# Performance work log

Measured on AMD Instinct MI355X. Metric: run time of the kernel, lower is better.

## Reference

```python
import jax, jax.numpy as jnp
import numpy as np

B, C, H, W = 16, 256, 64, 64
K, HID, ITERS, EPS = 4, 512, 3, 1e-8


def _ln(x, g, b, eps=1e-5):
    m = jnp.mean(x, axis=-1, keepdims=True)
    v = jnp.mean((x - m) ** 2, axis=-1, keepdims=True)
    return (x - m) * jax.lax.rsqrt(v + eps) * g + b


def setup_inputs() -> dict:
    key = jax.random.key(0)
    ks = jax.random.split(key, 24)

    def lin(k, o, i):
        lim = np.sqrt(6.0 / (o + i)).astype(np.float32)
        return jax.random.uniform(k, (o, i), jnp.float32, -lim, lim)

    return {
        "x": jax.random.normal(ks[0], (B, C, H, W), jnp.float32),
        "noise": jax.random.normal(ks[1], (B, K, C), jnp.float32),
        "slot_mu": jax.random.normal(ks[2], (1, 1, C), jnp.float32),
        "slot_log_sigma": jnp.zeros((1, 1, C), jnp.float32),
        "ln_in_g": jnp.ones((C,)), "ln_in_b": jnp.zeros((C,)),
        "ln_sl_g": jnp.ones((C,)), "ln_sl_b": jnp.zeros((C,)),
        "ln_mlp_g": jnp.ones((C,)), "ln_mlp_b": jnp.zeros((C,)),
        "Wq": lin(ks[3], C, C), "bq": jnp.zeros((C,)),
        "Wk": lin(ks[4], C, C), "bk": jnp.zeros((C,)),
        "Wv": lin(ks[5], C, C), "bv": jnp.zeros((C,)),
        "Wu": lin(ks[6], C, 2 * C), "bu": jnp.zeros((C,)),
        "W1": lin(ks[7], HID, C), "b1": jnp.zeros((HID,)),
        "W2": lin(ks[8], C, HID), "b2": jnp.zeros((C,)),
        "We1": lin(ks[9], C // 2, C), "be1": jnp.zeros((C // 2,)),
        "We2": lin(ks[10], 1, C // 2), "be2": jnp.zeros((1,)),
    }


def reference(x, noise, slot_mu, slot_log_sigma, ln_in_g, ln_in_b, ln_sl_g, ln_sl_b,
              ln_mlp_g, ln_mlp_b, Wq, bq, Wk, bk, Wv, bv, Wu, bu, W1, b1, W2, b2,
              We1, be1, We2, be2):
    # b c h w -> b (h w) c
    xn = x.reshape(B, C, H * W).transpose(0, 2, 1)
    xn = _ln(xn, ln_in_g, ln_in_b)
    # k, v depend only on xn; hoisted out of the loop (same math)
    k = jnp.einsum('bnc,dc->bnd', xn, Wk) + bk
    v = jnp.einsum('bnc,dc->bnd', xn, Wv) + bv
    scale = C ** (-0.5)
    slots = slot_mu + jnp.exp(slot_log_sigma) * noise
    for _ in range(ITERS):
        prev = slots
        s = _ln(slots, ln_sl_g, ln_sl_b)
        q = jnp.einsum('bkc,dc->bkd', s, Wq) + bq
        attn = jax.nn.softmax(jnp.einsum('bkc,bnc->bkn', q, k) * scale, axis=1)
        w = attn / (jnp.sum(attn, axis=-1, keepdims=True) + EPS)
        updates = jnp.einsum('bkn,bnc->bkc', w, v)
        combined = jnp.concatenate([prev, updates], axis=-1)  # (B,K,2C)
        slots = jnp.einsum('bkc,dc->bkd', combined, Wu) + bu + prev
        m = _ln(slots, ln_mlp_g, ln_mlp_b)
        h = jax.nn.gelu(jnp.einsum('bkc,hc->bkh', m, W1) + b1, approximate=False)
        slots = slots + jnp.einsum('bkh,ch->bkc', h, W2) + b2
    e = jax.nn.gelu(jnp.einsum('bkc,dc->bkd', slots, We1) + be1, approximate=False)
    slot_weights = jax.nn.sigmoid(jnp.einsum('bkd,od->bko', e, We2) + be2)[..., 0]
    return slots, slot_weights
```

## Files before the change

kernel.cpp:

```cpp
#include <hip/hip_runtime.h>
#include <math.h>

#define B_    16
#define C_    256
#define NPIX  4096
#define K_    4
#define HID_  512
#define ITERS_ 3
#define NROWS (B_*NPIX)
#define EPS_  1e-8f

__device__ __forceinline__ float gelu_f(float x) {
    return 0.5f * x * (1.0f + erff(x * 0.70710678118654752f));
}

__device__ __forceinline__ unsigned short f2bf(float x) {
    union { float f; unsigned u; } v; v.f = x;
    unsigned r = v.u + 0x7fffu + ((v.u >> 16) & 1u);
    return (unsigned short)(r >> 16);
}
__device__ __forceinline__ float bflo(unsigned u) {
    union { unsigned u; float f; } v; v.u = u << 16; return v.f;
}
__device__ __forceinline__ float bfhi(unsigned u) {
    union { unsigned u; float f; } v; v.u = u & 0xffff0000u; return v.f;
}
__device__ __forceinline__ float4 shfl_xor4(float4 v, int m) {
    v.x = __shfl_xor(v.x, m); v.y = __shfl_xor(v.y, m);
    v.z = __shfl_xor(v.z, m); v.w = __shfl_xor(v.w, m);
    return v;
}
__device__ __forceinline__ void fma4(float4& a, const float4 w, const float4 s) {
    a.x = fmaf(w.x, s.x, a.x); a.y = fmaf(w.y, s.y, a.y);
    a.z = fmaf(w.z, s.z, a.z); a.w = fmaf(w.w, s.w, a.w);
}
__device__ __forceinline__ float hsum4(const float4 a) {
    return (a.x + a.y) + (a.z + a.w);
}

__device__ __forceinline__ void redpair256t(float a, float b, int t, float* r8,
                                            float& o1, float& o2) {
    #pragma unroll
    for (int m = 1; m <= 32; m <<= 1) { a += __shfl_xor(a, m); b += __shfl_xor(b, m); }
    if ((t & 63) == 0) { r8[(t >> 6) * 2] = a; r8[(t >> 6) * 2 + 1] = b; }
    __syncthreads();
    o1 = r8[0] + r8[2] + r8[4] + r8[6];
    o2 = r8[1] + r8[3] + r8[5] + r8[7];
}

__global__ __launch_bounds__(256) void prep_pack_kernel(
    const float* __restrict__ Wu, const float* __restrict__ W1,
    const float* __restrict__ W2, const float* __restrict__ We1,
    const float* __restrict__ Wq, const float* __restrict__ bk,
    const float* __restrict__ bq,
    float4* __restrict__ WuC4, float4* __restrict__ W14,
    float4* __restrict__ W24, float4* __restrict__ We14,
    float* __restrict__ wqoff) {
    __shared__ float r4[4];
    int i = blockIdx.x * 256 + threadIdx.x;
    if (blockIdx.x == 352) {
        int c = threadIdx.x;
        float s = 0.f;
        for (int dd = 0; dd < 256; ++dd) s = fmaf(Wq[dd * 256 + c], bk[dd], s);
        wqoff[c] = s;
        float p = bq[c] * bk[c];
        #pragma unroll
        for (int m = 1; m <= 32; m <<= 1) p += __shfl_xor(p, m);
        if ((c & 63) == 0) r4[c >> 6] = p;
        __syncthreads();
        if (c == 0) wqoff[256] = r4[0] + r4[1] + r4[2] + r4[3];
        return;
    }
    if (i < 16384) {
        int c4 = i >> 8, dd = i & 255;
        WuC4[i] = *(const float4*)&Wu[dd * 512 + c4 * 4];
    } else if (i < 49152) {
        int j = i - 16384; int c4 = j >> 9, h = j & 511;
        W14[j] = *(const float4*)&W1[h * 256 + c4 * 4];
    } else if (i < 81920) {
        int j = i - 49152; int h4 = j >> 8, dd = j & 255;
        W24[j] = *(const float4*)&W2[dd * 512 + h4 * 4];
    } else {
        int j = i - 81920; int c4 = j >> 7, e = j & 127;
        We14[j] = *(const float4*)&We1[e * 256 + c4 * 4];
    }
}

__global__ __launch_bounds__(256) void prep_compose_kernel(
    const float* __restrict__ Wu, const float* __restrict__ Wv,
    const float* __restrict__ Wk, const float* __restrict__ Wq,
    const float* __restrict__ bv, const float* __restrict__ bq,
    float4* __restrict__ WuC4, float4* __restrict__ Wqk4,
    float* __restrict__ bv2, float* __restrict__ bqk) {
    __shared__ float wur[256], wkc[256];
    __shared__ float ldsA[256], ldsB[256];
    __shared__ float r1[4], r2[4];
    const int d = blockIdx.x, c = threadIdx.x;
    wur[c] = Wu[d * 512 + 256 + c];
    wkc[c] = Wk[c * 256 + d];
    __syncthreads();
    float a = 0.f, b = 0.f;
    #pragma unroll 4
    for (int e = 0; e < 256; ++e) {
        a = fmaf(wur[e], Wv[e * 256 + c], a);
        b = fmaf(wkc[e], Wq[e * 256 + c], b);
    }
    ldsA[c] = a; ldsB[c] = b;
    float p1 = wur[c] * bv[c], p2 = wkc[c] * bq[c];
    #pragma unroll
    for (int m = 1; m <= 32; m <<= 1) { p1 += __shfl_xor(p1, m); p2 += __shfl_xor(p2, m); }
    if ((c & 63) == 0) { r1[c >> 6] = p1; r2[c >> 6] = p2; }
    __syncthreads();
    if (c < 64) {
        float4 qa = { ldsA[4 * c], ldsA[4 * c + 1], ldsA[4 * c + 2], ldsA[4 * c + 3] };
        float4 qb = { ldsB[4 * c], ldsB[4 * c + 1], ldsB[4 * c + 2], ldsB[4 * c + 3] };
        WuC4[(64 + c) * 256 + d] = qa;
        Wqk4[c * 256 + d] = qb;
    }
    if (c == 0) {
        bv2[d] = r1[0] + r1[1] + r1[2] + r1[3];
        bqk[d] = r2[0] + r2[1] + r2[2] + r2[3];
    }
}

__global__ __launch_bounds__(256) void xn_fused_kernel(
    const float* __restrict__ x, const float* __restrict__ g, const float* __restrict__ bta,
    unsigned short* __restrict__ xnb) {
    __shared__ float tile[256][65];
    __shared__ float sg[256], sb[256];
    __shared__ float red1[256], red2[256];
    __shared__ float smean[64], srstd[64];
    const int tid = threadIdx.x;
    const int nt = blockIdx.x << 6, b = blockIdx.y;

    sg[tid] = g[tid]; sb[tid] = bta[tid];
    #pragma unroll
    for (int r = 0; r < 64; ++r) {
        int idx = tid + (r << 8);
        int c_l = idx >> 6, n_l = idx & 63;
        tile[c_l][n_l] = x[(size_t)(b * C_ + c_l) * NPIX + nt + n_l];
    }
    __syncthreads();
    {
        int cq = tid >> 6, n_l = tid & 63;
        float s = 0.f, s2 = 0.f;
        #pragma unroll 8
        for (int c = cq * 64; c < cq * 64 + 64; ++c) {
            float v = tile[c][n_l];
            s += v; s2 += v * v;
        }
        red1[tid] = s; red2[tid] = s2;
    }
    __syncthreads();
    if (tid < 64) {
        float s  = red1[tid] + red1[tid + 64] + red1[tid + 128] + red1[tid + 192];
        float s2 = red2[tid] + red2[tid + 64] + red2[tid + 128] + red2[tid + 192];
        float m = s * (1.0f / C_);
        smean[tid] = m;
        srstd[tid] = rsqrtf(s2 * (1.0f / C_) - m * m + 1e-5f);
    }
    __syncthreads();
    #pragma unroll
    for (int r = 0; r < 32; ++r) {
        int idx = tid + (r << 8);
        int n_l = idx >> 7, cp = idx & 127;
        int c0 = cp << 1;
        float mn = smean[n_l], rs = srstd[n_l];
        float v0 = (tile[c0][n_l] - mn) * rs * sg[c0] + sb[c0];
        float v1 = (tile[c0 + 1][n_l] - mn) * rs * sg[c0 + 1] + sb[c0 + 1];
        ushort2 o; o.x = f2bf(v0); o.y = f2bf(v1);
        *reinterpret_cast<ushort2*>(&xnb[((size_t)(b * NPIX + nt + n_l)) * C_ + c0]) = o;
    }
}


__global__ __launch_bounds__(256) void init_slots_kernel(
    const float* __restrict__ noise, const float* __restrict__ mu,
    const float* __restrict__ log_sigma,
    float* __restrict__ slots, float* __restrict__ usum, float* __restrict__ denom) {
    int t = threadIdx.x, r = blockIdx.x;
    float v = mu[t] + expf(log_sigma[t]) * noise[r * C_ + t];
    slots[r * C_ + t] = v;
    usum[r * C_ + t] = 0.f;
    if (t == 0) denom[r] = 0.f;
}

__global__ __launch_bounds__(256) void qt_kernel(
    const float* __restrict__ src,
    const float* __restrict__ g_sl, const float* __restrict__ b_sl,
    const float4* __restrict__ Wqk4, const float* __restrict__ bqk,
    const float* __restrict__ wqoff,
    float* __restrict__ qtbuf, float* __restrict__ qoffbuf) {
    __shared__ __align__(16) float snorm[256];
    __shared__ float pq[256];
    __shared__ float r8[8];
    const int t = threadIdx.x, dq = blockIdx.x, r = blockIdx.y;
    float v = src[r * C_ + t];
    float sm, s2;
    redpair256t(v, v * v, t, r8, sm, s2);
    float mean = sm * (1.f / C_);
    float rs = rsqrtf(s2 * (1.f / C_) - mean * mean + 1e-5f);
    snorm[t] = (v - mean) * rs * g_sl[t] + b_sl[t];
    __syncthreads();
    const float4* sn4 = (const float4*)snorm;
    const int dloc = t & 63, ks = t >> 6;
    const int d = dq * 64 + dloc;
    {
        float4 a0 = {0,0,0,0}, a1 = {0,0,0,0};
        int c4b = ks << 4;
        #pragma unroll
        for (int i = 0; i < 16; i += 2) {
            fma4(a0, Wqk4[(c4b + i) * 256 + d], sn4[c4b + i]);
            fma4(a1, Wqk4[(c4b + i + 1) * 256 + d], sn4[c4b + i + 1]);
        }
        pq[ks * 64 + dloc] = hsum4(a0) + hsum4(a1);
    }
    __syncthreads();
    if (t < 64) {
        float s = pq[t] + pq[64 + t] + pq[128 + t] + pq[192 + t];
        qtbuf[r * C_ + dq * 64 + t] = s + bqk[dq * 64 + t];
    }
    if (dq == 0) {
        float p = snorm[t] * wqoff[t];
        #pragma unroll
        for (int m = 1; m <= 32; m <<= 1) p += __shfl_xor(p, m);
        if ((t & 63) == 0) r8[t >> 6] = p;
        __syncthreads();
        if (t == 0) qoffbuf[r] = r8[0] + r8[1] + r8[2] + r8[3] + wqoff[256];
    }
}

__global__ __launch_bounds__(256) void upd_wu_kernel(
    const float* __restrict__ slots, const float* __restrict__ usum,
    const float* __restrict__ denom,
    const float4* __restrict__ WuC4, const float* __restrict__ bu,
    const float* __restrict__ bv2,
    float* __restrict__ nvbuf) {
    __shared__ __align__(16) float comb[512];
    __shared__ float pq[256];
    __shared__ float sden, sscale;
    const int t = threadIdx.x, dq = blockIdx.x, r = blockIdx.y;
    if (t == 0) { float dv = denom[r]; sden = dv + EPS_; sscale = dv / (dv + EPS_); }
    comb[t] = slots[r * C_ + t];
    float uv = usum[r * C_ + t];
    __syncthreads();
    comb[256 + t] = uv / sden;
    __syncthreads();
    const float4* cb4 = (const float4*)comb;
    const int dloc = t & 31, ks = t >> 5;
    const int d = dq * 32 + dloc;
    {
        float4 a0 = {0,0,0,0}, a1 = {0,0,0,0};
        int c4b = ks << 4;
        #pragma unroll
        for (int i = 0; i < 16; i += 2) {
            fma4(a0, WuC4[(c4b + i) * 256 + d], cb4[c4b + i]);
            fma4(a1, WuC4[(c4b + i + 1) * 256 + d], cb4[c4b + i + 1]);
        }
        pq[ks * 32 + dloc] = hsum4(a0) + hsum4(a1);
    }
    __syncthreads();
    if (t < 32) {
        int dd = dq * 32 + t;
        float s = 0.f;
        #pragma unroll
        for (int i = 0; i < 8; ++i) s += pq[i * 32 + t];
        nvbuf[r * C_ + dd] = s + bu[dd] + comb[dd] + sscale * bv2[dd];
    }
}

__global__ __launch_bounds__(256) void upd_w1_kernel(
    const float* __restrict__ nvbuf,
    const float* __restrict__ g_mlp, const float* __restrict__ b_mlp,
    const float4* __restrict__ W14, const float* __restrict__ b1,
    float* __restrict__ hbuf, float* __restrict__ usum, float* __restrict__ denom) {
    __shared__ __align__(16) float mrow[256];
    __shared__ float pq[256];
    __shared__ float r8[8];
    const int t = threadIdx.x, hq = blockIdx.x, r = blockIdx.y;
    float nv = nvbuf[r * C_ + t];
    float sm, s2;
    redpair256t(nv, nv * nv, t, r8, sm, s2);
    float mean = sm * (1.f / C_);
    float rs = rsqrtf(s2 * (1.f / C_) - mean * mean + 1e-5f);
    mrow[t] = (nv - mean) * rs * g_mlp[t] + b_mlp[t];
    if (hq == 0) {
        usum[r * C_ + t] = 0.f;
        if (t == 0) denom[r] = 0.f;
    }
    __syncthreads();
    const float4* m4 = (const float4*)mrow;
    const int hloc = t & 63, ks = t >> 6;
    const int h = hq * 64 + hloc;
    {
        float4 a0 = {0,0,0,0}, a1 = {0,0,0,0};
        int c4b = ks << 4;
        #pragma unroll
        for (int i = 0; i < 16; i += 2) {
            fma4(a0, W14[(c4b + i) * 512 + h], m4[c4b + i]);
            fma4(a1, W14[(c4b + i + 1) * 512 + h], m4[c4b + i + 1]);
        }
        pq[ks * 64 + hloc] = hsum4(a0) + hsum4(a1);
    }
    __syncthreads();
    if (t < 64) {
        float s = pq[t] + pq[64 + t] + pq[128 + t] + pq[192 + t];
        hbuf[r * HID_ + hq * 64 + t] = gelu_f(s + b1[hq * 64 + t]);
    }
}

__global__ __launch_bounds__(256) void upd_w2_kernel(
    const float* __restrict__ nvbuf, const float* __restrict__ hbuf,
    const float4* __restrict__ W24, const float* __restrict__ b2,
    float* __restrict__ dst) {
    __shared__ __align__(16) float hrow[512];
    __shared__ float pq[256];
    const int t = threadIdx.x, dq = blockIdx.x, r = blockIdx.y;
    hrow[t] = hbuf[r * HID_ + t];
    hrow[256 + t] = hbuf[r * HID_ + 256 + t];
    __syncthreads();
    const float4* h4 = (const float4*)hrow;
    const int dloc = t & 31, ks = t >> 5;
    const int d = dq * 32 + dloc;
    {
        float4 a0 = {0,0,0,0}, a1 = {0,0,0,0};
        int h4b = ks << 4;
        #pragma unroll
        for (int i = 0; i < 16; i += 2) {
            fma4(a0, W24[(h4b + i) * 256 + d], h4[h4b + i]);
            fma4(a1, W24[(h4b + i + 1) * 256 + d], h4[h4b + i + 1]);
        }
        pq[ks * 32 + dloc] = hsum4(a0) + hsum4(a1);
    }
    __syncthreads();
    if (t < 32) {
        int dd = dq * 32 + t;
        float s = 0.f;
        #pragma unroll
        for (int i = 0; i < 8; ++i) s += pq[i * 32 + t];
        dst[r * C_ + dd] = nvbuf[r * C_ + dd] + s + b2[dd];
    }
}

__global__ __launch_bounds__(256) void head_kernel(
    const float* __restrict__ ovbuf,
    const float4* __restrict__ We14, const float* __restrict__ be1,
    const float* __restrict__ We2, const float* __restrict__ be2,
    float* __restrict__ out) {
    __shared__ __align__(16) float mrow[256];
    __shared__ float pq[256];
    __shared__ float erow[128];
    __shared__ float r4[4];
    const int t = threadIdx.x, r = blockIdx.x;
    mrow[t] = ovbuf[r * C_ + t];
    __syncthreads();
    const float4* m4 = (const float4*)mrow;
    const int e = t & 127, o2 = t >> 7;
    {
        float4 a0 = {0,0,0,0}, a1 = {0,0,0,0};
        int c4b = o2 << 5;
        #pragma unroll
        for (int i = 0; i < 32; i += 2) {
            fma4(a0, We14[(c4b + i) * 128 + e], m4[c4b + i]);
            fma4(a1, We14[(c4b + i + 1) * 128 + e], m4[c4b + i + 1]);
        }
        pq[o2 * 128 + e] = hsum4(a0) + hsum4(a1);
    }
    __syncthreads();
    if (t < 128) erow[t] = gelu_f(pq[t] + pq[128 + t] + be1[t]);
    __syncthreads();
    if (t < 64) {
        float p = We2[t] * erow[t] + We2[t + 64] * erow[t + 64];
        #pragma unroll
        for (int m = 1; m <= 32; m <<= 1) p += __shfl_xor(p, m);
        if (t == 0) { r4[0] = p; }
    }
    __syncthreads();
    if (t == 0) out[B_ * K_ * C_ + r] = 1.0f / (1.0f + expf(-(r4[0] + be2[0])));
}

__global__ __launch_bounds__(256) void attn_fused_kernel(
    const float* __restrict__ qtbuf, const float* __restrict__ qoffbuf,
    const unsigned short* __restrict__ xnb,
    float* __restrict__ usum, float* __restrict__ denom) {
    __shared__ float4 qT[264];
    __shared__ float attns[K_][64];
    __shared__ float upd_s[K_][256];
    __shared__ float asw[4][4];
    __shared__ float4 qo_s;

    const int tid = threadIdx.x;
    const int b = blockIdx.y;
    const int chunk = blockIdx.x;
    const int n0 = chunk << 6;
    const int wave = tid >> 6, lane = tid & 63;

    {
        int c = tid;
        float4 qv;
        qv.x = qtbuf[b * 1024 + c];
        qv.y = qtbuf[b * 1024 + 256 + c];
        qv.z = qtbuf[b * 1024 + 512 + c];
        qv.w = qtbuf[b * 1024 + 768 + c];
        qT[c + (c >> 5)] = qv;
        if (tid == 0) qo_s = *(const float4*)&qoffbuf[b * 4];
    }
    __syncthreads();

    const int cpart = tid & 7;
    const int npair = tid >> 3;
    const int c0 = cpart << 5;
    float4 acc0 = {0.f, 0.f, 0.f, 0.f}, acc1 = {0.f, 0.f, 0.f, 0.f};
    const unsigned short* kbase = xnb + ((size_t)b * NPIX + n0 + npair * 2) * C_ + c0;
    #pragma unroll
    for (int j = 0; j < 4; ++j) {
        uint4 k0 = *reinterpret_cast<const uint4*>(kbase + j * 8);
        uint4 k1 = *reinterpret_cast<const uint4*>(kbase + C_ + j * 8);
        const unsigned kw0[4] = {k0.x, k0.y, k0.z, k0.w};
        const unsigned kw1[4] = {k1.x, k1.y, k1.z, k1.w};
        #pragma unroll
        for (int jj = 0; jj < 4; ++jj) {
            int cidx = c0 + j * 8 + jj * 2 + cpart;
            float4 qa = qT[cidx];
            float4 qb = qT[cidx + 1];
            float f00 = bflo(kw0[jj]), f01 = bfhi(kw0[jj]);
            float f10 = bflo(kw1[jj]), f11 = bfhi(kw1[jj]);
            acc0.x += f00 * qa.x + f01 * qb.x;  acc0.y += f00 * qa.y + f01 * qb.y;
            acc0.z += f00 * qa.z + f01 * qb.z;  acc0.w += f00 * qa.w + f01 * qb.w;
            acc1.x += f10 * qa.x + f11 * qb.x;  acc1.y += f10 * qa.y + f11 * qb.y;
            acc1.z += f10 * qa.z + f11 * qb.z;  acc1.w += f10 * qa.w + f11 * qb.w;
        }
    }
    #pragma unroll
    for (int m = 1; m <= 4; m <<= 1) {
        acc0 = acc0 + shfl_xor4(acc0, m);
        acc1 = acc1 + shfl_xor4(acc1, m);
    }
    float4 w0, w1;
    {
        float4 l = (acc0 + qo_s) * 0.0625f;
        float mx = fmaxf(fmaxf(l.x, l.y), fmaxf(l.z, l.w));
        w0.x = expf(l.x - mx); w0.y = expf(l.y - mx);
        w0.z = expf(l.z - mx); w0.w = expf(l.w - mx);
        float inv = 1.0f / (w0.x + w0.y + w0.z + w0.w);
        w0 = w0 * inv;
        l = (acc1 + qo_s) * 0.0625f;
        mx = fmaxf(fmaxf(l.x, l.y), fmaxf(l.z, l.w));
        w1.x = expf(l.x - mx); w1.y = expf(l.y - mx);
        w1.z = expf(l.z - mx); w1.w = expf(l.w - mx);
        inv = 1.0f / (w1.x + w1.y + w1.z + w1.w);
        w1 = w1 * inv;
    }
    if (cpart == 0) {
        int n_l = npair * 2;
        attns[0][n_l] = w0.x; attns[1][n_l] = w0.y; attns[2][n_l] = w0.z; attns[3][n_l] = w0.w;
        attns[0][n_l + 1] = w1.x; attns[1][n_l + 1] = w1.y;
        attns[2][n_l + 1] = w1.z; attns[3][n_l + 1] = w1.w;
    }
    float4 ws = w0 + w1;
    #pragma unroll
    for (int m = 8; m <= 32; m <<= 1) ws = ws + shfl_xor4(ws, m);
    if (lane == 0) {
        asw[wave][0] = ws.x; asw[wave][1] = ws.y; asw[wave][2] = ws.z; asw[wave][3] = ws.w;
    }
    __syncthreads();
    if (tid < 4)
        atomicAdd(&denom[b * 4 + tid],
                  asw[0][tid] + asw[1][tid] + asw[2][tid] + asw[3][tid]);

    const int h = wave >> 1;
    const int chalf = (wave & 1) << 7;
    const int c = chalf + lane * 2;
    float a0[K_] = {0.f, 0.f, 0.f, 0.f};
    float a1[K_] = {0.f, 0.f, 0.f, 0.f};
    const unsigned short* vbase = xnb + ((size_t)b * NPIX + n0 + h * 32) * C_ + c;
    #pragma unroll 4
    for (int nn = 0; nn < 32; ++nn) {
        unsigned vv = *reinterpret_cast<const unsigned*>(vbase + (size_t)nn * C_);
        float v0 = bflo(vv), v1 = bfhi(vv);
        int n_l = h * 32 + nn;
        float q0 = attns[0][n_l], q1 = attns[1][n_l], q2 = attns[2][n_l], q3 = attns[3][n_l];
        a0[0] = fmaf(q0, v0, a0[0]); a1[0] = fmaf(q0, v1, a1[0]);
        a0[1] = fmaf(q1, v0, a0[1]); a1[1] = fmaf(q1, v1, a1[1]);
        a0[2] = fmaf(q2, v0, a0[2]); a1[2] = fmaf(q2, v1, a1[2]);
        a0[3] = fmaf(q3, v0, a0[3]); a1[3] = fmaf(q3, v1, a1[3]);
    }
    __syncthreads();
    if (h == 0) {
        #pragma unroll
        for (int k = 0; k < K_; ++k) { upd_s[k][c] = a0[k]; upd_s[k][c + 1] = a1[k]; }
    }
    __syncthreads();
    if (h == 1) {
        #pragma unroll
        for (int k = 0; k < K_; ++k) { upd_s[k][c] += a0[k]; upd_s[k][c + 1] += a1[k]; }
    }
    __syncthreads();
    #pragma unroll
    for (int k = 0; k < K_; ++k)
        atomicAdd(&usum[((size_t)b * K_ + k) * 256 + tid], upd_s[k][tid]);
}

extern "C" void kernel_launch(void* const* d_in, const int* in_sizes, int n_in,
                              void* d_out, int out_size, void* d_ws, size_t ws_size,
                              hipStream_t stream) {
    (void)in_sizes; (void)n_in; (void)out_size; (void)ws_size;
    const float* x        = (const float*)d_in[0];
    const float* noise    = (const float*)d_in[1];
    const float* slot_mu  = (const float*)d_in[2];
    const float* slot_ls  = (const float*)d_in[3];
    const float* ln_in_g  = (const float*)d_in[4];
    const float* ln_in_b  = (const float*)d_in[5];
    const float* ln_sl_g  = (const float*)d_in[6];
    const float* ln_sl_b  = (const float*)d_in[7];
    const float* ln_mlp_g = (const float*)d_in[8];
    const float* ln_mlp_b = (const float*)d_in[9];
    const float* Wq = (const float*)d_in[10];
    const float* bq = (const float*)d_in[11];
    const float* Wk = (const float*)d_in[12];
    const float* bk = (const float*)d_in[13];
    const float* Wv = (const float*)d_in[14];
    const float* bv = (const float*)d_in[15];
    const float* Wu = (const float*)d_in[16];
    const float* bu = (const float*)d_in[17];
    const float* W1 = (const float*)d_in[18];
    const float* b1 = (const float*)d_in[19];
    const float* W2 = (const float*)d_in[20];
    const float* b2 = (const float*)d_in[21];
    const float* We1 = (const float*)d_in[22];
    const float* be1 = (const float*)d_in[23];
    const float* We2 = (const float*)d_in[24];
    const float* be2 = (const float*)d_in[25];
    float* out = (float*)d_out;

    char* ws = (char*)d_ws;
    unsigned short* xnb = (unsigned short*)ws;
    float4* WuC4 = (float4*)(xnb + (size_t)NROWS * C_);
    float4* W14  = WuC4 + 32768;
    float4* W24  = W14 + 32768;
    float4* We14 = W24 + 32768;
    float4* Wqk4 = We14 + 8192;
    float* bv2   = (float*)(Wqk4 + 16384);
    float* bqk   = bv2 + 256;
    float* wqoff = bqk + 256;
    float* slots = wqoff + 260;
    float* qtbuf = slots + B_ * K_ * C_;
    float* qoffb = qtbuf + B_ * K_ * C_;
    float* usum  = qoffb + B_ * K_;
    float* denom = usum + B_ * K_ * C_;
    float* nvbuf = denom + B_ * K_;
    float* hbuf  = nvbuf + B_ * K_ * C_;

    prep_pack_kernel<<<353, 256, 0, stream>>>(Wu, W1, W2, We1, Wq, bk, bq,
                                              WuC4, W14, W24, We14, wqoff);
    prep_compose_kernel<<<256, 256, 0, stream>>>(Wu, Wv, Wk, Wq, bv, bq,
                                                 WuC4, Wqk4, bv2, bqk);
    xn_fused_kernel<<<dim3(64, 16), 256, 0, stream>>>(x, ln_in_g, ln_in_b, xnb);
    init_slots_kernel<<<B_ * K_, 256, 0, stream>>>(noise, slot_mu, slot_ls,
                                                   slots, usum, denom);
    qt_kernel<<<dim3(4, B_ * K_), 256, 0, stream>>>(slots, ln_sl_g, ln_sl_b,
                                                    Wqk4, bqk, wqoff, qtbuf, qoffb);
    for (int it = 0; it < ITERS_; ++it) {
        attn_fused_kernel<<<dim3(64, 16), 256, 0, stream>>>(qtbuf, qoffb, xnb,
                                                            usum, denom);
        upd_wu_kernel<<<dim3(8, B_ * K_), 256, 0, stream>>>(slots, usum, denom,
                                                            WuC4, bu, bv2, nvbuf);
        upd_w1_kernel<<<dim3(8, B_ * K_), 256, 0, stream>>>(nvbuf, ln_mlp_g, ln_mlp_b,
                                                            W14, b1, hbuf, usum, denom);
        upd_w2_kernel<<<dim3(8, B_ * K_), 256, 0, stream>>>(
            nvbuf, hbuf, W24, b2, (it < ITERS_ - 1) ? slots : out);
        if (it < ITERS_ - 1)
            qt_kernel<<<dim3(4, B_ * K_), 256, 0, stream>>>(slots, ln_sl_g, ln_sl_b,
                                                            Wqk4, bqk, wqoff, qtbuf, qoffb);
    }
    head_kernel<<<B_ * K_, 256, 0, stream>>>(out, We14, be1, We2, be2, out);
}
```

Measured before the change: 299.0 us.

## Fuse slot-update chain into one kernel, merge prep kernels, retile attention and LN

Merges the two weight-prep kernels into one launch and folds slot init into the first q-projection kernel. Replaces the per-iteration Wu/W1/W2/qt/head kernel chain with a single upd_full kernel that does the update, MLP, next query and final head. It double-buffers slots and usum/denom so the accumulators can be cleared without racing. The attention kernel now runs on half as many blocks, each looping over more pixels. The input layernorm uses 512 threads and accumulates its statistics while loading. This cuts launch count and intermediate global round-trips, but each fused block recomputes the update redundantly across 2 blocks and uses less parallelism per row.

```diff
diff --git a/kernel.cpp b/kernel.cpp
--- a/kernel.cpp
+++ b/kernel.cpp
@@ -48,54 +48,53 @@
     o2 = r8[1] + r8[3] + r8[5] + r8[7];
 }
 
-__global__ __launch_bounds__(256) void prep_pack_kernel(
+__global__ __launch_bounds__(256) void prep_all_kernel(
     const float* __restrict__ Wu, const float* __restrict__ W1,
     const float* __restrict__ W2, const float* __restrict__ We1,
-    const float* __restrict__ Wq, const float* __restrict__ bk,
-    const float* __restrict__ bq,
+    const float* __restrict__ Wq, const float* __restrict__ Wk,
+    const float* __restrict__ Wv,
+    const float* __restrict__ bk, const float* __restrict__ bq,
+    const float* __restrict__ bv,
     float4* __restrict__ WuC4, float4* __restrict__ W14,
     float4* __restrict__ W24, float4* __restrict__ We14,
-    float* __restrict__ wqoff) {
-    __shared__ float r4[4];
-    int i = blockIdx.x * 256 + threadIdx.x;
-    if (blockIdx.x == 352) {
-        int c = threadIdx.x;
-        float s = 0.f;
-        for (int dd = 0; dd < 256; ++dd) s = fmaf(Wq[dd * 256 + c], bk[dd], s);
-        wqoff[c] = s;
-        float p = bq[c] * bk[c];
-        #pragma unroll
-        for (int m = 1; m <= 32; m <<= 1) p += __shfl_xor(p, m);
-        if ((c & 63) == 0) r4[c >> 6] = p;
-        __syncthreads();
-        if (c == 0) wqoff[256] = r4[0] + r4[1] + r4[2] + r4[3];
+    float4* __restrict__ Wqk4,
+    float* __restrict__ bv2, float* __restrict__ bqk, float* __restrict__ wqoff) {
+    const int role = blockIdx.x;
+    if (role < 353) {
+        __shared__ float r4[4];
+        if (role == 352) {
+            int c = threadIdx.x;
+            float s = 0.f;
+            for (int dd = 0; dd < 256; ++dd) s = fmaf(Wq[dd * 256 + c], bk[dd], s);
+            wqoff[c] = s;
+            float p = bq[c] * bk[c];
+            #pragma unroll
+            for (int m = 1; m <= 32; m <<= 1) p += __shfl_xor(p, m);
+            if ((c & 63) == 0) r4[c >> 6] = p;
+            __syncthreads();
+            if (c == 0) wqoff[256] = r4[0] + r4[1] + r4[2] + r4[3];
+            return;
+        }
+        int i = role * 256 + threadIdx.x;
+        if (i < 16384) {
+            int c4 = i >> 8, dd = i & 255;
+            WuC4[i] = *(const float4*)&Wu[dd * 512 + c4 * 4];
+        } else if (i < 49152) {
+            int j = i - 16384; int c4 = j >> 9, h = j & 511;
+            W14[j] = *(const float4*)&W1[h * 256 + c4 * 4];
+        } else if (i < 81920) {
+            int j = i - 49152; int h4 = j >> 8, dd = j & 255;
+            W24[j] = *(const float4*)&W2[dd * 512 + h4 * 4];
+        } else {
+            int j = i - 81920; int c4 = j >> 7, e = j & 127;
+            We14[j] = *(const float4*)&We1[e * 256 + c4 * 4];
+        }
         return;
     }
-    if (i < 16384) {
-        int c4 = i >> 8, dd = i & 255;
-        WuC4[i] = *(const float4*)&Wu[dd * 512 + c4 * 4];
-    } else if (i < 49152) {
-        int j = i - 16384; int c4 = j >> 9, h = j & 511;
-        W14[j] = *(const float4*)&W1[h * 256 + c4 * 4];
-    } else if (i < 81920) {
-        int j = i - 49152; int h4 = j >> 8, dd = j & 255;
-        W24[j] = *(const float4*)&W2[dd * 512 + h4 * 4];
-    } else {
-        int j = i - 81920; int c4 = j >> 7, e = j & 127;
-        We14[j] = *(const float4*)&We1[e * 256 + c4 * 4];
-    }
-}
-
-__global__ __launch_bounds__(256) void prep_compose_kernel(
-    const float* __restrict__ Wu, const float* __restrict__ Wv,
-    const float* __restrict__ Wk, const float* __restrict__ Wq,
-    const float* __restrict__ bv, const float* __restrict__ bq,
-    float4* __restrict__ WuC4, float4* __restrict__ Wqk4,
-    float* __restrict__ bv2, float* __restrict__ bqk) {
     __shared__ float wur[256], wkc[256];
     __shared__ float ldsA[256], ldsB[256];
     __shared__ float r1[4], r2[4];
-    const int d = blockIdx.x, c = threadIdx.x;
+    const int d = role - 353, c = threadIdx.x;
     wur[c] = Wu[d * 512 + 256 + c];
     wkc[c] = Wk[c * 256 + d];
     __syncthreads();
@@ -123,46 +122,40 @@
     }
 }
 
-__global__ __launch_bounds__(256) void xn_fused_kernel(
+__global__ __launch_bounds__(512) void xn_fused_kernel(
     const float* __restrict__ x, const float* __restrict__ g, const float* __restrict__ bta,
     unsigned short* __restrict__ xnb) {
     __shared__ float tile[256][65];
     __shared__ float sg[256], sb[256];
-    __shared__ float red1[256], red2[256];
+    __shared__ float red1[512], red2[512];
     __shared__ float smean[64], srstd[64];
     const int tid = threadIdx.x;
     const int nt = blockIdx.x << 6, b = blockIdx.y;
 
-    sg[tid] = g[tid]; sb[tid] = bta[tid];
-    #pragma unroll
-    for (int r = 0; r < 64; ++r) {
-        int idx = tid + (r << 8);
-        int c_l = idx >> 6, n_l = idx & 63;
-        tile[c_l][n_l] = x[(size_t)(b * C_ + c_l) * NPIX + nt + n_l];
-    }
-    __syncthreads();
-    {
-        int cq = tid >> 6, n_l = tid & 63;
-        float s = 0.f, s2 = 0.f;
-        #pragma unroll 8
-        for (int c = cq * 64; c < cq * 64 + 64; ++c) {
-            float v = tile[c][n_l];
-            s += v; s2 += v * v;
-        }
-        red1[tid] = s; red2[tid] = s2;
-    }
-    __syncthreads();
-    if (tid < 64) {
-        float s  = red1[tid] + red1[tid + 64] + red1[tid + 128] + red1[tid + 192];
-        float s2 = red2[tid] + red2[tid + 64] + red2[tid + 128] + red2[tid + 192];
-        float m = s * (1.0f / C_);
-        smean[tid] = m;
-        srstd[tid] = rsqrtf(s2 * (1.0f / C_) - m * m + 1e-5f);
-    }
-    __syncthreads();
+    if (tid < 256) { sg[tid] = g[tid]; sb[tid] = bta[tid]; }
+    float s = 0.f, s2 = 0.f;
     #pragma unroll
     for (int r = 0; r < 32; ++r) {
-        int idx = tid + (r << 8);
+        int idx = tid + (r << 9);
+        int c_l = idx >> 6, n_l = idx & 63;
+        float v = x[(size_t)(b * C_ + c_l) * NPIX + nt + n_l];
+        tile[c_l][n_l] = v;
+        s += v; s2 += v * v;
+    }
+    red1[tid] = s; red2[tid] = s2;
+    __syncthreads();
+    if (tid < 64) {
+        float a = 0.f, a2 = 0.f;
+        #pragma unroll
+        for (int j = 0; j < 8; ++j) { a += red1[tid + 64 * j]; a2 += red2[tid + 64 * j]; }
+        float m = a * (1.0f / C_);
+        smean[tid] = m;
+        srstd[tid] = rsqrtf(a2 * (1.0f / C_) - m * m + 1e-5f);
+    }
+    __syncthreads();
+    #pragma unroll
+    for (int r = 0; r < 16; ++r) {
+        int idx = tid + (r << 9);
         int n_l = idx >> 7, cp = idx & 127;
         int c0 = cp << 1;
         float mn = smean[n_l], rs = srstd[n_l];
@@ -173,55 +166,48 @@
     }
 }
 
-
-__global__ __launch_bounds__(256) void init_slots_kernel(
+__global__ __launch_bounds__(256) void initqt_kernel(
     const float* __restrict__ noise, const float* __restrict__ mu,
     const float* __restrict__ log_sigma,
-    float* __restrict__ slots, float* __restrict__ usum, float* __restrict__ denom) {
-    int t = threadIdx.x, r = blockIdx.x;
-    float v = mu[t] + expf(log_sigma[t]) * noise[r * C_ + t];
-    slots[r * C_ + t] = v;
-    usum[r * C_ + t] = 0.f;
-    if (t == 0) denom[r] = 0.f;
-}
-
-__global__ __launch_bounds__(256) void qt_kernel(
-    const float* __restrict__ src,
     const float* __restrict__ g_sl, const float* __restrict__ b_sl,
     const float4* __restrict__ Wqk4, const float* __restrict__ bqk,
     const float* __restrict__ wqoff,
-    float* __restrict__ qtbuf, float* __restrict__ qoffbuf) {
-    __shared__ __align__(16) float snorm[256];
+    float* __restrict__ slots, float* __restrict__ qtbuf, float* __restrict__ qoffbuf,
+    float* __restrict__ usum0, float* __restrict__ denom0) {
+    __shared__ __align__(16) float mrow[256];
     __shared__ float pq[256];
     __shared__ float r8[8];
     const int t = threadIdx.x, dq = blockIdx.x, r = blockIdx.y;
-    float v = src[r * C_ + t];
+    float v = mu[t] + expf(log_sigma[t]) * noise[r * C_ + t];
+    if (dq == 0) {
+        slots[r * C_ + t] = v;
+        usum0[r * C_ + t] = 0.f;
+        if (t == 0) denom0[r] = 0.f;
+    }
     float sm, s2;
     redpair256t(v, v * v, t, r8, sm, s2);
     float mean = sm * (1.f / C_);
     float rs = rsqrtf(s2 * (1.f / C_) - mean * mean + 1e-5f);
-    snorm[t] = (v - mean) * rs * g_sl[t] + b_sl[t];
-    __syncthreads();
-    const float4* sn4 = (const float4*)snorm;
-    const int dloc = t & 63, ks = t >> 6;
-    const int d = dq * 64 + dloc;
+    mrow[t] = (v - mean) * rs * g_sl[t] + b_sl[t];
+    __syncthreads();
+    const float4* sn4 = (const float4*)mrow;
+    const int dloc = t & 127, ks = t >> 7;
+    const int dout = dq * 128 + dloc;
     {
         float4 a0 = {0,0,0,0}, a1 = {0,0,0,0};
-        int c4b = ks << 4;
-        #pragma unroll
-        for (int i = 0; i < 16; i += 2) {
-            fma4(a0, Wqk4[(c4b + i) * 256 + d], sn4[c4b + i]);
-            fma4(a1, Wqk4[(c4b + i + 1) * 256 + d], sn4[c4b + i + 1]);
-        }
-        pq[ks * 64 + dloc] = hsum4(a0) + hsum4(a1);
-    }
-    __syncthreads();
-    if (t < 64) {
-        float s = pq[t] + pq[64 + t] + pq[128 + t] + pq[192 + t];
-        qtbuf[r * C_ + dq * 64 + t] = s + bqk[dq * 64 + t];
-    }
+        int c4b = ks << 5;
+        #pragma unroll
+        for (int i = 0; i < 32; i += 2) {
+            fma4(a0, Wqk4[(c4b + i) * 256 + dout], sn4[c4b + i]);
+            fma4(a1, Wqk4[(c4b + i + 1) * 256 + dout], sn4[c4b + i + 1]);
+        }
+        pq[ks * 128 + dloc] = hsum4(a0) + hsum4(a1);
+    }
+    __syncthreads();
+    if (t < 128)
+        qtbuf[r * C_ + dq * 128 + t] = pq[t] + pq[128 + t] + bqk[dq * 128 + t];
     if (dq == 0) {
-        float p = snorm[t] * wqoff[t];
+        float p = mrow[t] * wqoff[t];
         #pragma unroll
         for (int m = 1; m <= 32; m <<= 1) p += __shfl_xor(p, m);
         if ((t & 63) == 0) r8[t >> 6] = p;
@@ -230,153 +216,148 @@
     }
 }
 
-__global__ __launch_bounds__(256) void upd_wu_kernel(
-    const float* __restrict__ slots, const float* __restrict__ usum,
-    const float* __restrict__ denom,
+__global__ __launch_bounds__(256) void upd_full_kernel(
+    const float* __restrict__ slots_in,
+    const float* __restrict__ usum_cur, const float* __restrict__ denom_cur,
+    float* __restrict__ usum_nxt, float* __restrict__ denom_nxt,
     const float4* __restrict__ WuC4, const float* __restrict__ bu,
     const float* __restrict__ bv2,
-    float* __restrict__ nvbuf) {
-    __shared__ __align__(16) float comb[512];
-    __shared__ float pq[256];
-    __shared__ float sden, sscale;
-    const int t = threadIdx.x, dq = blockIdx.x, r = blockIdx.y;
-    if (t == 0) { float dv = denom[r]; sden = dv + EPS_; sscale = dv / (dv + EPS_); }
-    comb[t] = slots[r * C_ + t];
-    float uv = usum[r * C_ + t];
-    __syncthreads();
-    comb[256 + t] = uv / sden;
-    __syncthreads();
-    const float4* cb4 = (const float4*)comb;
-    const int dloc = t & 31, ks = t >> 5;
-    const int d = dq * 32 + dloc;
-    {
-        float4 a0 = {0,0,0,0}, a1 = {0,0,0,0};
-        int c4b = ks << 4;
-        #pragma unroll
-        for (int i = 0; i < 16; i += 2) {
-            fma4(a0, WuC4[(c4b + i) * 256 + d], cb4[c4b + i]);
-            fma4(a1, WuC4[(c4b + i + 1) * 256 + d], cb4[c4b + i + 1]);
-        }
-        pq[ks * 32 + dloc] = hsum4(a0) + hsum4(a1);
-    }
-    __syncthreads();
-    if (t < 32) {
-        int dd = dq * 32 + t;
-        float s = 0.f;
-        #pragma unroll
-        for (int i = 0; i < 8; ++i) s += pq[i * 32 + t];
-        nvbuf[r * C_ + dd] = s + bu[dd] + comb[dd] + sscale * bv2[dd];
-    }
-}
-
-__global__ __launch_bounds__(256) void upd_w1_kernel(
-    const float* __restrict__ nvbuf,
     const float* __restrict__ g_mlp, const float* __restrict__ b_mlp,
     const float4* __restrict__ W14, const float* __restrict__ b1,
-    float* __restrict__ hbuf, float* __restrict__ usum, float* __restrict__ denom) {
-    __shared__ __align__(16) float mrow[256];
-    __shared__ float pq[256];
-    __shared__ float r8[8];
-    const int t = threadIdx.x, hq = blockIdx.x, r = blockIdx.y;
-    float nv = nvbuf[r * C_ + t];
-    float sm, s2;
-    redpair256t(nv, nv * nv, t, r8, sm, s2);
-    float mean = sm * (1.f / C_);
-    float rs = rsqrtf(s2 * (1.f / C_) - mean * mean + 1e-5f);
-    mrow[t] = (nv - mean) * rs * g_mlp[t] + b_mlp[t];
-    if (hq == 0) {
-        usum[r * C_ + t] = 0.f;
-        if (t == 0) denom[r] = 0.f;
-    }
-    __syncthreads();
-    const float4* m4 = (const float4*)mrow;
-    const int hloc = t & 63, ks = t >> 6;
-    const int h = hq * 64 + hloc;
-    {
-        float4 a0 = {0,0,0,0}, a1 = {0,0,0,0};
-        int c4b = ks << 4;
-        #pragma unroll
-        for (int i = 0; i < 16; i += 2) {
-            fma4(a0, W14[(c4b + i) * 512 + h], m4[c4b + i]);
-            fma4(a1, W14[(c4b + i + 1) * 512 + h], m4[c4b + i + 1]);
-        }
-        pq[ks * 64 + hloc] = hsum4(a0) + hsum4(a1);
-    }
-    __syncthreads();
-    if (t < 64) {
-        float s = pq[t] + pq[64 + t] + pq[128 + t] + pq[192 + t];
-        hbuf[r * HID_ + hq * 64 + t] = gelu_f(s + b1[hq * 64 + t]);
-    }
-}
-
-__global__ __launch_bounds__(256) void upd_w2_kernel(
-    const float* __restrict__ nvbuf, const float* __restrict__ hbuf,
     const float4* __restrict__ W24, const float* __restrict__ b2,
-    float* __restrict__ dst) {
-    __shared__ __align__(16) float hrow[512];
-    __shared__ float pq[256];
-    const int t = threadIdx.x, dq = blockIdx.x, r = blockIdx.y;
-    hrow[t] = hbuf[r * HID_ + t];
-    hrow[256 + t] = hbuf[r * HID_ + 256 + t];
-    __syncthreads();
-    const float4* h4 = (const float4*)hrow;
-    const int dloc = t & 31, ks = t >> 5;
-    const int d = dq * 32 + dloc;
-    {
-        float4 a0 = {0,0,0,0}, a1 = {0,0,0,0};
-        int h4b = ks << 4;
-        #pragma unroll
-        for (int i = 0; i < 16; i += 2) {
-            fma4(a0, W24[(h4b + i) * 256 + d], h4[h4b + i]);
-            fma4(a1, W24[(h4b + i + 1) * 256 + d], h4[h4b + i + 1]);
-        }
-        pq[ks * 32 + dloc] = hsum4(a0) + hsum4(a1);
-    }
-    __syncthreads();
-    if (t < 32) {
-        int dd = dq * 32 + t;
-        float s = 0.f;
-        #pragma unroll
-        for (int i = 0; i < 8; ++i) s += pq[i * 32 + t];
-        dst[r * C_ + dd] = nvbuf[r * C_ + dd] + s + b2[dd];
-    }
-}
-
-__global__ __launch_bounds__(256) void head_kernel(
-    const float* __restrict__ ovbuf,
+    const float* __restrict__ g_sl, const float* __restrict__ b_sl,
+    const float4* __restrict__ Wqk4, const float* __restrict__ bqk,
+    const float* __restrict__ wqoff,
+    float* __restrict__ qtbuf, float* __restrict__ qoffbuf,
+    float* __restrict__ dst,
     const float4* __restrict__ We14, const float* __restrict__ be1,
     const float* __restrict__ We2, const float* __restrict__ be2,
-    float* __restrict__ out) {
+    float* __restrict__ out, int final_it) {
+    __shared__ __align__(16) float comb[512];
     __shared__ __align__(16) float mrow[256];
     __shared__ float pq[256];
     __shared__ float erow[128];
-    __shared__ float r4[4];
-    const int t = threadIdx.x, r = blockIdx.x;
-    mrow[t] = ovbuf[r * C_ + t];
-    __syncthreads();
-    const float4* m4 = (const float4*)mrow;
-    const int e = t & 127, o2 = t >> 7;
+    __shared__ float r8[8];
+    __shared__ float sden, sscale;
+    const int t = threadIdx.x, dq = blockIdx.x, r = blockIdx.y;
+
+    float prev = slots_in[r * C_ + t];
+    float uv = usum_cur[r * C_ + t];
+    if (!final_it && dq == 0) {
+        usum_nxt[r * C_ + t] = 0.f;
+        if (t == 0) denom_nxt[r] = 0.f;
+    }
+    if (t == 0) { float dv = denom_cur[r]; sden = dv + EPS_; sscale = dv / (dv + EPS_); }
+    comb[t] = prev;
+    __syncthreads();
+    comb[256 + t] = uv / sden;
+    __syncthreads();
+    float nv;
     {
+        const float4* cb4 = (const float4*)comb;
         float4 a0 = {0,0,0,0}, a1 = {0,0,0,0};
-        int c4b = o2 << 5;
-        #pragma unroll
-        for (int i = 0; i < 32; i += 2) {
-            fma4(a0, We14[(c4b + i) * 128 + e], m4[c4b + i]);
-            fma4(a1, We14[(c4b + i + 1) * 128 + e], m4[c4b + i + 1]);
-        }
-        pq[o2 * 128 + e] = hsum4(a0) + hsum4(a1);
-    }
-    __syncthreads();
-    if (t < 128) erow[t] = gelu_f(pq[t] + pq[128 + t] + be1[t]);
-    __syncthreads();
-    if (t < 64) {
-        float p = We2[t] * erow[t] + We2[t + 64] * erow[t + 64];
-        #pragma unroll
-        for (int m = 1; m <= 32; m <<= 1) p += __shfl_xor(p, m);
-        if (t == 0) { r4[0] = p; }
-    }
-    __syncthreads();
-    if (t == 0) out[B_ * K_ * C_ + r] = 1.0f / (1.0f + expf(-(r4[0] + be2[0])));
+        #pragma unroll 8
+        for (int c4 = 0; c4 < 128; c4 += 2) {
+            fma4(a0, WuC4[c4 * 256 + t], cb4[c4]);
+            fma4(a1, WuC4[(c4 + 1) * 256 + t], cb4[c4 + 1]);
+        }
+        nv = hsum4(a0) + hsum4(a1) + bu[t] + prev + sscale * bv2[t];
+    }
+    {
+        float sm, s2;
+        redpair256t(nv, nv * nv, t, r8, sm, s2);
+        float mean = sm * (1.f / C_);
+        float rs = rsqrtf(s2 * (1.f / C_) - mean * mean + 1e-5f);
+        mrow[t] = (nv - mean) * rs * g_mlp[t] + b_mlp[t];
+    }
+    __syncthreads();
+    {
+        const float4* m4 = (const float4*)mrow;
+        float4 a0 = {0,0,0,0}, a1 = {0,0,0,0}, a2 = {0,0,0,0}, a3 = {0,0,0,0};
+        #pragma unroll 4
+        for (int c4 = 0; c4 < 64; c4 += 2) {
+            float4 s0 = m4[c4], s1 = m4[c4 + 1];
+            fma4(a0, W14[c4 * 512 + t], s0);
+            fma4(a1, W14[(c4 + 1) * 512 + t], s1);
+            fma4(a2, W14[c4 * 512 + t + 256], s0);
+            fma4(a3, W14[(c4 + 1) * 512 + t + 256], s1);
+        }
+        float h0 = gelu_f(hsum4(a0) + hsum4(a1) + b1[t]);
+        float h1 = gelu_f(hsum4(a2) + hsum4(a3) + b1[t + 256]);
+        __syncthreads();
+        comb[t] = h0; comb[256 + t] = h1;
+    }
+    __syncthreads();
+    float ov;
+    {
+        const float4* h4 = (const float4*)comb;
+        float4 a0 = {0,0,0,0}, a1 = {0,0,0,0};
+        #pragma unroll 8
+        for (int h4i = 0; h4i < 128; h4i += 2) {
+            fma4(a0, W24[h4i * 256 + t], h4[h4i]);
+            fma4(a1, W24[(h4i + 1) * 256 + t], h4[h4i + 1]);
+        }
+        ov = nv + hsum4(a0) + hsum4(a1) + b2[t];
+    }
+    if ((t >> 7) == dq) dst[r * C_ + t] = ov;
+    if (!final_it) {
+        float sm, s2;
+        redpair256t(ov, ov * ov, t, r8, sm, s2);
+        float mean = sm * (1.f / C_);
+        float rs = rsqrtf(s2 * (1.f / C_) - mean * mean + 1e-5f);
+        mrow[t] = (ov - mean) * rs * g_sl[t] + b_sl[t];
+        __syncthreads();
+        const float4* sn4 = (const float4*)mrow;
+        const int dloc = t & 127, ks = t >> 7;
+        const int dout = dq * 128 + dloc;
+        {
+            float4 a0 = {0,0,0,0}, a1 = {0,0,0,0};
+            int c4b = ks << 5;
+            #pragma unroll
+            for (int i = 0; i < 32; i += 2) {
+                fma4(a0, Wqk4[(c4b + i) * 256 + dout], sn4[c4b + i]);
+                fma4(a1, Wqk4[(c4b + i + 1) * 256 + dout], sn4[c4b + i + 1]);
+            }
+            pq[ks * 128 + dloc] = hsum4(a0) + hsum4(a1);
+        }
+        __syncthreads();
+        if (t < 128)
+            qtbuf[r * C_ + dq * 128 + t] = pq[t] + pq[128 + t] + bqk[dq * 128 + t];
+        if (dq == 0) {
+            float p = mrow[t] * wqoff[t];
+            #pragma unroll
+            for (int m = 1; m <= 32; m <<= 1) p += __shfl_xor(p, m);
+            if ((t & 63) == 0) r8[t >> 6] = p;
+            __syncthreads();
+            if (t == 0) qoffbuf[r] = r8[0] + r8[1] + r8[2] + r8[3] + wqoff[256];
+        }
+    } else if (dq == 0) {
+        mrow[t] = ov;
+        __syncthreads();
+        const float4* m4 = (const float4*)mrow;
+        const int e = t & 127, o2 = t >> 7;
+        {
+            float4 a0 = {0,0,0,0}, a1 = {0,0,0,0};
+            int c4b = o2 << 5;
+            #pragma unroll
+            for (int i = 0; i < 32; i += 2) {
+                fma4(a0, We14[(c4b + i) * 128 + e], m4[c4b + i]);
+                fma4(a1, We14[(c4b + i + 1) * 128 + e], m4[c4b + i + 1]);
+            }
+            pq[o2 * 128 + e] = hsum4(a0) + hsum4(a1);
+        }
+        __syncthreads();
+        if (t < 128) erow[t] = gelu_f(pq[t] + pq[128 + t] + be1[t]);
+        __syncthreads();
+        if (t < 64) {
+            float p = We2[t] * erow[t] + We2[t + 64] * erow[t + 64];
+            #pragma unroll
+            for (int m = 1; m <= 32; m <<= 1) p += __shfl_xor(p, m);
+            if (t == 0) r8[0] = p;
+        }
+        __syncthreads();
+        if (t == 0) out[B_ * K_ * C_ + r] = 1.0f / (1.0f + expf(-(r8[0] + be2[0])));
+    }
 }
 
 __global__ __launch_bounds__(256) void attn_fused_kernel(
@@ -391,8 +372,7 @@
 
     const int tid = threadIdx.x;
     const int b = blockIdx.y;
-    const int chunk = blockIdx.x;
-    const int n0 = chunk << 6;
+    const int n0 = blockIdx.x << 7;
     const int wave = tid >> 6, lane = tid & 63;
 
     {
@@ -410,90 +390,97 @@
     const int cpart = tid & 7;
     const int npair = tid >> 3;
     const int c0 = cpart << 5;
-    float4 acc0 = {0.f, 0.f, 0.f, 0.f}, acc1 = {0.f, 0.f, 0.f, 0.f};
-    const unsigned short* kbase = xnb + ((size_t)b * NPIX + n0 + npair * 2) * C_ + c0;
+    const int h = wave >> 1;
+    const int vc = ((wave & 1) << 7) + lane * 2;
+    float va0[K_] = {0.f, 0.f, 0.f, 0.f};
+    float va1[K_] = {0.f, 0.f, 0.f, 0.f};
+    float4 wacc = {0.f, 0.f, 0.f, 0.f};
+
+    for (int sc = 0; sc < 2; ++sc) {
+        const int nb = n0 + (sc << 6);
+        float4 acc0 = {0.f, 0.f, 0.f, 0.f}, acc1 = {0.f, 0.f, 0.f, 0.f};
+        const unsigned short* kbase = xnb + ((size_t)b * NPIX + nb + npair * 2) * C_ + c0;
+        #pragma unroll
+        for (int j = 0; j < 4; ++j) {
+            uint4 k0 = *reinterpret_cast<const uint4*>(kbase + j * 8);
+            uint4 k1 = *reinterpret_cast<const uint4*>(kbase + C_ + j * 8);
+            const unsigned kw0[4] = {k0.x, k0.y, k0.z, k0.w};
+            const unsigned kw1[4] = {k1.x, k1.y, k1.z, k1.w};
+            #pragma unroll
+            for (int jj = 0; jj < 4; ++jj) {
+                int cidx = c0 + j * 8 + jj * 2 + cpart;
+                float4 qa = qT[cidx];
+                float4 qb = qT[cidx + 1];
+                float f00 = bflo(kw0[jj]), f01 = bfhi(kw0[jj]);
+                float f10 = bflo(kw1[jj]), f11 = bfhi(kw1[jj]);
+                acc0.x += f00 * qa.x + f01 * qb.x;  acc0.y += f00 * qa.y + f01 * qb.y;
+                acc0.z += f00 * qa.z + f01 * qb.z;  acc0.w += f00 * qa.w + f01 * qb.w;
+                acc1.x += f10 * qa.x + f11 * qb.x;  acc1.y += f10 * qa.y + f11 * qb.y;
+                acc1.z += f10 * qa.z + f11 * qb.z;  acc1.w += f10 * qa.w + f11 * qb.w;
+            }
+        }
+        #pragma unroll
+        for (int m = 1; m <= 4; m <<= 1) {
+            acc0 = acc0 + shfl_xor4(acc0, m);
+            acc1 = acc1 + shfl_xor4(acc1, m);
+        }
+        float4 w0, w1;
+        {
+            float4 l = (acc0 + qo_s) * 0.0625f;
+            float mx = fmaxf(fmaxf(l.x, l.y), fmaxf(l.z, l.w));
+            w0.x = expf(l.x - mx); w0.y = expf(l.y - mx);
+            w0.z = expf(l.z - mx); w0.w = expf(l.w - mx);
+            float inv = 1.0f / (w0.x + w0.y + w0.z + w0.w);
+            w0 = w0 * inv;
+            l = (acc1 + qo_s) * 0.0625f;
+            mx = fmaxf(fmaxf(l.x, l.y), fmaxf(l.z, l.w));
+            w1.x = expf(l.x - mx); w1.y = expf(l.y - mx);
+            w1.z = expf(l.z - mx); w1.w = expf(l.w - mx);
+            inv = 1.0f / (w1.x + w1.y + w1.z + w1.w);
+            w1 = w1 * inv;
+        }
+        if (cpart == 0) {
+            int n_l = npair * 2;
+            attns[0][n_l] = w0.x; attns[1][n_l] = w0.y;
+            attns[2][n_l] = w0.z; attns[3][n_l] = w0.w;
+            attns[0][n_l + 1] = w1.x; attns[1][n_l + 1] = w1.y;
+            attns[2][n_l + 1] = w1.z; attns[3][n_l + 1] = w1.w;
+        }
+        wacc = wacc + w0 + w1;
+        __syncthreads();
+        const unsigned short* vbase = xnb + ((size_t)b * NPIX + nb + h * 32) * C_ + vc;
+        #pragma unroll 4
+        for (int nn = 0; nn < 32; ++nn) {
+            unsigned vv = *reinterpret_cast<const unsigned*>(vbase + (size_t)nn * C_);
+            float v0 = bflo(vv), v1 = bfhi(vv);
+            int n_l = h * 32 + nn;
+            float q0 = attns[0][n_l], q1 = attns[1][n_l];
+            float q2 = attns[2][n_l], q3 = attns[3][n_l];
+            va0[0] = fmaf(q0, v0, va0[0]); va1[0] = fmaf(q0, v1, va1[0]);
+            va0[1] = fmaf(q1, v0, va0[1]); va1[1] = fmaf(q1, v1, va1[1]);
+            va0[2] = fmaf(q2, v0, va0[2]); va1[2] = fmaf(q2, v1, va1[2]);
+            va0[3] = fmaf(q3, v0, va0[3]); va1[3] = fmaf(q3, v1, va1[3]);
+        }
+        __syncthreads();
+    }
     #pragma unroll
-    for (int j = 0; j < 4; ++j) {
-        uint4 k0 = *reinterpret_cast<const uint4*>(kbase + j * 8);
-        uint4 k1 = *reinterpret_cast<const uint4*>(kbase + C_ + j * 8);
-        const unsigned kw0[4] = {k0.x, k0.y, k0.z, k0.w};
-        const unsigned kw1[4] = {k1.x, k1.y, k1.z, k1.w};
-        #pragma unroll
-        for (int jj = 0; jj < 4; ++jj) {
-            int cidx = c0 + j * 8 + jj * 2 + cpart;
-            float4 qa = qT[cidx];
-            float4 qb = qT[cidx + 1];
-            float f00 = bflo(kw0[jj]), f01 = bfhi(kw0[jj]);
-            float f10 = bflo(kw1[jj]), f11 = bfhi(kw1[jj]);
-            acc0.x += f00 * qa.x + f01 * qb.x;  acc0.y += f00 * qa.y + f01 * qb.y;
-            acc0.z += f00 * qa.z + f01 * qb.z;  acc0.w += f00 * qa.w + f01 * qb.w;
-            acc1.x += f10 * qa.x + f11 * qb.x;  acc1.y += f10 * qa.y + f11 * qb.y;
-            acc1.z += f10 * qa.z + f11 * qb.z;  acc1.w += f10 * qa.w + f11 * qb.w;
-        }
-    }
-    #pragma unroll
-    for (int m = 1; m <= 4; m <<= 1) {
-        acc0 = acc0 + shfl_xor4(acc0, m);
-        acc1 = acc1 + shfl_xor4(acc1, m);
-    }
-    float4 w0, w1;
-    {
-        float4 l = (acc0 + qo_s) * 0.0625f;
-        float mx = fmaxf(fmaxf(l.x, l.y), fmaxf(l.z, l.w));
-        w0.x = expf(l.x - mx); w0.y = expf(l.y - mx);
-        w0.z = expf(l.z - mx); w0.w = expf(l.w - mx);
-        float inv = 1.0f / (w0.x + w0.y + w0.z + w0.w);
-        w0 = w0 * inv;
-        l = (acc1 + qo_s) * 0.0625f;
-        mx = fmaxf(fmaxf(l.x, l.y), fmaxf(l.z, l.w));
-        w1.x = expf(l.x - mx); w1.y = expf(l.y - mx);
-        w1.z = expf(l.z - mx); w1.w = expf(l.w - mx);
-        inv = 1.0f / (w1.x + w1.y + w1.z + w1.w);
-        w1 = w1 * inv;
-    }
-    if (cpart == 0) {
-        int n_l = npair * 2;
-        attns[0][n_l] = w0.x; attns[1][n_l] = w0.y; attns[2][n_l] = w0.z; attns[3][n_l] = w0.w;
-        attns[0][n_l + 1] = w1.x; attns[1][n_l + 1] = w1.y;
-        attns[2][n_l + 1] = w1.z; attns[3][n_l + 1] = w1.w;
-    }
-    float4 ws = w0 + w1;
-    #pragma unroll
-    for (int m = 8; m <= 32; m <<= 1) ws = ws + shfl_xor4(ws, m);
+    for (int m = 8; m <= 32; m <<= 1) wacc = wacc + shfl_xor4(wacc, m);
     if (lane == 0) {
-        asw[wave][0] = ws.x; asw[wave][1] = ws.y; asw[wave][2] = ws.z; asw[wave][3] = ws.w;
+        asw[wave][0] = wacc.x; asw[wave][1] = wacc.y;
+        asw[wave][2] = wacc.z; asw[wave][3] = wacc.w;
     }
     __syncthreads();
     if (tid < 4)
         atomicAdd(&denom[b * 4 + tid],
                   asw[0][tid] + asw[1][tid] + asw[2][tid] + asw[3][tid]);
-
-    const int h = wave >> 1;
-    const int chalf = (wave & 1) << 7;
-    const int c = chalf + lane * 2;
-    float a0[K_] = {0.f, 0.f, 0.f, 0.f};
-    float a1[K_] = {0.f, 0.f, 0.f, 0.f};
-    const unsigned short* vbase = xnb + ((size_t)b * NPIX + n0 + h * 32) * C_ + c;
-    #pragma unroll 4
-    for (int nn = 0; nn < 32; ++nn) {
-        unsigned vv = *reinterpret_cast<const unsigned*>(vbase + (size_t)nn * C_);
-        float v0 = bflo(vv), v1 = bfhi(vv);
-        int n_l = h * 32 + nn;
-        float q0 = attns[0][n_l], q1 = attns[1][n_l], q2 = attns[2][n_l], q3 = attns[3][n_l];
-        a0[0] = fmaf(q0, v0, a0[0]); a1[0] = fmaf(q0, v1, a1[0]);
-        a0[1] = fmaf(q1, v0, a0[1]); a1[1] = fmaf(q1, v1, a1[1]);
-        a0[2] = fmaf(q2, v0, a0[2]); a1[2] = fmaf(q2, v1, a1[2]);
-        a0[3] = fmaf(q3, v0, a0[3]); a1[3] = fmaf(q3, v1, a1[3]);
-    }
-    __syncthreads();
     if (h == 0) {
         #pragma unroll
-        for (int k = 0; k < K_; ++k) { upd_s[k][c] = a0[k]; upd_s[k][c + 1] = a1[k]; }
+        for (int k = 0; k < K_; ++k) { upd_s[k][vc] = va0[k]; upd_s[k][vc + 1] = va1[k]; }
     }
     __syncthreads();
     if (h == 1) {
         #pragma unroll
-        for (int k = 0; k < K_; ++k) { upd_s[k][c] += a0[k]; upd_s[k][c + 1] += a1[k]; }
+        for (int k = 0; k < K_; ++k) { upd_s[k][vc] += va0[k]; upd_s[k][vc + 1] += va1[k]; }
     }
     __syncthreads();
     #pragma unroll
@@ -540,38 +527,38 @@
     float4* W24  = W14 + 32768;
     float4* We14 = W24 + 32768;
     float4* Wqk4 = We14 + 8192;
-    float* bv2   = (float*)(Wqk4 + 16384);
-    float* bqk   = bv2 + 256;
-    float* wqoff = bqk + 256;
-    float* slots = wqoff + 260;
-    float* qtbuf = slots + B_ * K_ * C_;
-    float* qoffb = qtbuf + B_ * K_ * C_;
-    float* usum  = qoffb + B_ * K_;
-    float* denom = usum + B_ * K_ * C_;
-    float* nvbuf = denom + B_ * K_;
-    float* hbuf  = nvbuf + B_ * K_ * C_;
-
-    prep_pack_kernel<<<353, 256, 0, stream>>>(Wu, W1, W2, We1, Wq, bk, bq,
-                                              WuC4, W14, W24, We14, wqoff);
-    prep_compose_kernel<<<256, 256, 0, stream>>>(Wu, Wv, Wk, Wq, bv, bq,
-                                                 WuC4, Wqk4, bv2, bqk);
-    xn_fused_kernel<<<dim3(64, 16), 256, 0, stream>>>(x, ln_in_g, ln_in_b, xnb);
-    init_slots_kernel<<<B_ * K_, 256, 0, stream>>>(noise, slot_mu, slot_ls,
-                                                   slots, usum, denom);
-    qt_kernel<<<dim3(4, B_ * K_), 256, 0, stream>>>(slots, ln_sl_g, ln_sl_b,
-                                                    Wqk4, bqk, wqoff, qtbuf, qoffb);
+    float* bv2    = (float*)(Wqk4 + 16384);
+    float* bqk    = bv2 + 256;
+    float* wqoff  = bqk + 256;
+    float* slots0 = wqoff + 260;
+    float* slots1 = slots0 + B_ * K_ * C_;
+    float* qtbuf  = slots1 + B_ * K_ * C_;
+    float* qoffb  = qtbuf + B_ * K_ * C_;
+    float* usum0  = qoffb + B_ * K_;
+    float* denom0 = usum0 + B_ * K_ * C_;
+    float* usum1  = denom0 + B_ * K_;
+    float* denom1 = usum1 + B_ * K_ * C_;
+
+    prep_all_kernel<<<609, 256, 0, stream>>>(Wu, W1, W2, We1, Wq, Wk, Wv, bk, bq, bv,
+                                             WuC4, W14, W24, We14, Wqk4,
+                                             bv2, bqk, wqoff);
+    xn_fused_kernel<<<dim3(64, 16), 512, 0, stream>>>(x, ln_in_g, ln_in_b, xnb);
+    initqt_kernel<<<dim3(2, B_ * K_), 256, 0, stream>>>(noise, slot_mu, slot_ls,
+                                                        ln_sl_g, ln_sl_b, Wqk4, bqk, wqoff,
+                                                        slots0, qtbuf, qoffb, usum0, denom0);
     for (int it = 0; it < ITERS_; ++it) {
-        attn_fused_kernel<<<dim3(64, 16), 256, 0, stream>>>(qtbuf, qoffb, xnb,
-                                                            usum, denom);
-        upd_wu_kernel<<<dim3(8, B_ * K_), 256, 0, stream>>>(slots, usum, denom,
-                                                            WuC4, bu, bv2, nvbuf);
-        upd_w1_kernel<<<dim3(8, B_ * K_), 256, 0, stream>>>(nvbuf, ln_mlp_g, ln_mlp_b,
-                                                            W14, b1, hbuf, usum, denom);
-        upd_w2_kernel<<<dim3(8, B_ * K_), 256, 0, stream>>>(
-            nvbuf, hbuf, W24, b2, (it < ITERS_ - 1) ? slots : out);
-        if (it < ITERS_ - 1)
-            qt_kernel<<<dim3(4, B_ * K_), 256, 0, stream>>>(slots, ln_sl_g, ln_sl_b,
-                                                            Wqk4, bqk, wqoff, qtbuf, qoffb);
-    }
-    head_kernel<<<B_ * K_, 256, 0, stream>>>(out, We14, be1, We2, be2, out);
-}
+        const int fin = (it == ITERS_ - 1);
+        float* usA = (it & 1) ? usum1 : usum0;
+        float* dnA = (it & 1) ? denom1 : denom0;
+        float* usB = (it & 1) ? usum0 : usum1;
+        float* dnB = (it & 1) ? denom0 : denom1;
+        const float* sin = (it & 1) ? slots1 : slots0;
+        float* sout = fin ? out : ((it & 1) ? slots0 : slots1);
+        attn_fused_kernel<<<dim3(32, 16), 256, 0, stream>>>(qtbuf, qoffb, xnb, usA, dnA);
+        upd_full_kernel<<<dim3(2, B_ * K_), 256, 0, stream>>>(
+            sin, usA, dnA, usB, dnB,
+            WuC4, bu, bv2, ln_mlp_g, ln_mlp_b, W14, b1, W24, b2,
+            ln_sl_g, ln_sl_b, Wqk4, bqk, wqoff, qtbuf, qoffb,
+            sout, We14, be1, We2, be2, out, fin);
+    }
+}
```

Measured after the change: 362.5 us. 1.21x slower.
